# Optimization experiments

Hardware: AMD Instinct MI355X
Metric: run time of the kernel (lower is better)

Reference implementation:

```python
import jax, jax.numpy as jnp
import numpy as np

B, S, D = 4, 2048, 1024
DFF = 512
E = 16
TOP_K = 2
N_SHARED = 2
FUSED_DFF = DFF * N_SHARED


def setup_inputs() -> dict:
    key = jax.random.key(0)
    ks = jax.random.split(key, 16)
    sc_d = 1.0 / np.sqrt(D)
    sc_f = 1.0 / np.sqrt(DFF)
    sc_sf = 1.0 / np.sqrt(FUSED_DFF)
    inp = {
        "x": jax.random.normal(ks[0], (B, S, D), dtype=jnp.float32),
        "gate_w": jax.random.uniform(ks[1], (E, D), dtype=jnp.float32, minval=-sc_d, maxval=sc_d),
        "expert_bias": jnp.zeros((E,), dtype=jnp.float32),
        # routed experts (SwiGLU): w1,w3: [E, DFF, D], w2: [E, D, DFF]
        "w1": jax.random.uniform(ks[2], (E, DFF, D), dtype=jnp.float32, minval=-sc_d, maxval=sc_d),
        "b1": jax.random.uniform(ks[3], (E, DFF), dtype=jnp.float32, minval=-sc_d, maxval=sc_d),
        "w3": jax.random.uniform(ks[4], (E, DFF, D), dtype=jnp.float32, minval=-sc_d, maxval=sc_d),
        "b3": jax.random.uniform(ks[5], (E, DFF), dtype=jnp.float32, minval=-sc_d, maxval=sc_d),
        "w2": jax.random.uniform(ks[6], (E, D, DFF), dtype=jnp.float32, minval=-sc_f, maxval=sc_f),
        "b2": jax.random.uniform(ks[7], (E, D), dtype=jnp.float32, minval=-sc_f, maxval=sc_f),
        # fused shared experts: d_model -> 2*d_ff -> d_model
        "sw1": jax.random.uniform(ks[8], (FUSED_DFF, D), dtype=jnp.float32, minval=-sc_d, maxval=sc_d),
        "sb1": jax.random.uniform(ks[9], (FUSED_DFF,), dtype=jnp.float32, minval=-sc_d, maxval=sc_d),
        "sw3": jax.random.uniform(ks[10], (FUSED_DFF, D), dtype=jnp.float32, minval=-sc_d, maxval=sc_d),
        "sb3": jax.random.uniform(ks[11], (FUSED_DFF,), dtype=jnp.float32, minval=-sc_d, maxval=sc_d),
        "sw2": jax.random.uniform(ks[12], (D, FUSED_DFF), dtype=jnp.float32, minval=-sc_sf, maxval=sc_sf),
        "sb2": jax.random.uniform(ks[13], (D,), dtype=jnp.float32, minval=-sc_sf, maxval=sc_sf),
    }
    return inp


def reference(x, gate_w, expert_bias, w1, b1, w2, b2, w3, b3,
              sw1, sb1, sw2, sb2, sw3, sb3):
    Bv, Sv, Dv = x.shape
    xf = x.reshape(-1, Dv)                                  # [T, D]
    # --- Gate (sigmoid scores, top-k over bias-adjusted logits) ---
    logits = xf @ gate_w.T                                  # [T, E]
    scores = jax.nn.sigmoid(logits)
    biased = logits + expert_bias.astype(logits.dtype)[None, :]
    _, topk_idx = jax.lax.top_k(biased, TOP_K)              # [T, K]
    topk_w = jnp.take_along_axis(scores, topk_idx, axis=-1) # [T, K]
    topk_w = topk_w / (topk_w.sum(-1, keepdims=True) + 1e-10)
    # dense per-token per-expert combine weight (zero for unselected) [T, E]
    gatew = (jax.nn.one_hot(topk_idx, E, dtype=xf.dtype) * topk_w[..., None]).sum(1)
    # --- Routed experts: equivalent to sort/dispatch/grouped-GEMM/combine ---
    y = jnp.zeros_like(xf)
    for e in range(E):
        h = jax.nn.silu(xf @ w1[e].T + b1[e]) * (xf @ w3[e].T + b3[e])  # [T, DFF]
        y = y + gatew[:, e:e + 1] * (h @ w2[e].T + b2[e])
    # --- Fused shared experts ---
    hs = jax.nn.silu(xf @ sw1.T + sb1) * (xf @ sw3.T + sb3)             # [T, 2*DFF]
    y = y + hs @ sw2.T + sb2
    return y.reshape(Bv, Sv, Dv)
```

## Files before the change

kernel.cpp:

```cpp
#include <hip/hip_runtime.h>
#include <cstdint>
#include <cstddef>

#define DEV static __device__ __forceinline__

constexpr int TT   = 8192;
constexpr int DD   = 1024;
constexpr int DFF  = 512;
constexpr int NE   = 16;
constexpr int FDFF = 1024;
constexpr int NSLOT = TT * 2;
constexpr int NSLOT_PAD = NSLOT + NE * 128;
constexpr int MAXT = NSLOT / 128 + NE;
constexpr int HB   = 64;

constexpr size_t XB_OFF   = 0;
constexpr size_t HS_OFF   = XB_OFF  + (size_t)TT * DD * 2;
constexpr size_t HR_OFF   = HS_OFF  + (size_t)TT * FDFF * 2;
constexpr size_t YR_OFF   = HR_OFF  + (size_t)NSLOT_PAD * DFF * 2;
constexpr size_t W1B_OFF  = YR_OFF  + (size_t)NSLOT_PAD * DD * 2;
constexpr size_t W3B_OFF  = W1B_OFF + (size_t)NE * DFF * DD * 2;
constexpr size_t W2B_OFF  = W3B_OFF + (size_t)NE * DFF * DD * 2;
constexpr size_t SW1B_OFF = W2B_OFF + (size_t)NE * DD * DFF * 2;
constexpr size_t SW3B_OFF = SW1B_OFF + (size_t)FDFF * DD * 2;
constexpr size_t SW2B_OFF = SW3B_OFF + (size_t)FDFF * DD * 2;
constexpr size_t TKI_OFF  = SW2B_OFF + (size_t)DD * FDFF * 2;
constexpr size_t TKW_OFF  = TKI_OFF + (size_t)NSLOT * 4;
constexpr size_t STOK_OFF = TKW_OFF + (size_t)NSLOT * 4;
constexpr size_t TSL_OFF  = STOK_OFF + (size_t)NSLOT_PAD * 4;
constexpr size_t LRK_OFF  = TSL_OFF + (size_t)NSLOT * 4;
constexpr size_t BCN_OFF  = LRK_OFF + (size_t)NSLOT * 4;
constexpr size_t BB_OFF   = BCN_OFF + (size_t)HB * NE * 4;
constexpr size_t OFS_OFF  = BB_OFF + (size_t)HB * NE * 4;
constexpr size_t TEX_OFF  = OFS_OFF + 128;
constexpr size_t TM0_OFF  = TEX_OFF + (size_t)MAXT * 4;

typedef __bf16 bf16x8 __attribute__((ext_vector_type(8)));
typedef float  floatx4 __attribute__((ext_vector_type(4)));
typedef unsigned short u16t;

DEV unsigned f2bf2(float lo, float hi) {
    unsigned a = __builtin_bit_cast(unsigned, lo);
    unsigned b = __builtin_bit_cast(unsigned, hi);
    a += 0x7FFFu + ((a >> 16) & 1u);
    b += 0x7FFFu + ((b >> 16) & 1u);
    return (a >> 16) | (b & 0xFFFF0000u);
}
DEV u16t f2bf1(float f) {
    unsigned u = __builtin_bit_cast(unsigned, f);
    u += 0x7FFFu + ((u >> 16) & 1u);
    return (u16t)(u >> 16);
}
DEV float bf2f(u16t v) {
    return __builtin_bit_cast(float, ((unsigned)v) << 16);
}
DEV uint4 pack8(float4 a, float4 b) {
    uint4 r;
    r.x = f2bf2(a.x, a.y); r.y = f2bf2(a.z, a.w);
    r.z = f2bf2(b.x, b.y); r.w = f2bf2(b.z, b.w);
    return r;
}
DEV floatx4 mfma16(bf16x8 a, bf16x8 b, floatx4 c) {
    return __builtin_amdgcn_mfma_f32_16x16x32_bf16(a, b, c, 0, 0, 0);
}
DEV void glds16(const u16t* g, u16t* l) {
    __builtin_amdgcn_global_load_lds(
        (const __attribute__((address_space(1))) unsigned int*)g,
        (__attribute__((address_space(3))) unsigned int*)l, 16, 0, 0);
}
DEV float dot4(float4 a, float4 b) { return a.x*b.x + a.y*b.y + a.z*b.z + a.w*b.w; }

__global__ __launch_bounds__(256) void k_cvtw(
        const float* __restrict__ w1, const float* __restrict__ w3, const float* __restrict__ w2,
        const float* __restrict__ sw1, const float* __restrict__ sw3, const float* __restrict__ sw2,
        u16t* __restrict__ w1b, u16t* __restrict__ w3b, u16t* __restrict__ w2b,
        u16t* __restrict__ sw1b, u16t* __restrict__ sw3b, u16t* __restrict__ sw2b) {
    int b = blockIdx.x;
    const float* src; u16t* dst; size_t base;
    if      (b < 4096)  { src = w1;  dst = w1b;  base = (size_t)b * 2048; }
    else if (b < 8192)  { src = w3;  dst = w3b;  base = (size_t)(b - 4096) * 2048; }
    else if (b < 12288) { src = w2;  dst = w2b;  base = (size_t)(b - 8192) * 2048; }
    else if (b < 12800) { src = sw1; dst = sw1b; base = (size_t)(b - 12288) * 2048; }
    else if (b < 13312) { src = sw3; dst = sw3b; base = (size_t)(b - 12800) * 2048; }
    else                { src = sw2; dst = sw2b; base = (size_t)(b - 13312) * 2048; }
    size_t i = base + (size_t)threadIdx.x * 8;
    float4 a = *(const float4*)(src + i);
    float4 c = *(const float4*)(src + i + 4);
    *(uint4*)(dst + i) = pack8(a, c);
}

__global__ __launch_bounds__(256) void k_gate(const float* __restrict__ x,
                                              const float* __restrict__ gw,
                                              const float* __restrict__ eb,
                                              int* __restrict__ tki, float* __restrict__ tkw,
                                              u16t* __restrict__ xb) {
    const int tid = threadIdx.x;
    const int wave = tid >> 6, lane = tid & 63;
    const int tok0 = blockIdx.x * 16 + wave * 4;
    float acc[4][16];
#pragma unroll
    for (int t = 0; t < 4; t++)
#pragma unroll
        for (int e = 0; e < 16; e++) acc[t][e] = 0.f;
#pragma unroll
    for (int i = 0; i < 4; i++) {
        const int d = i * 256 + lane * 4;
        float4 xv[4];
#pragma unroll
        for (int t = 0; t < 4; t++) xv[t] = *(const float4*)(x + (size_t)(tok0 + t) * DD + d);
#pragma unroll
        for (int t = 0; t < 4; t++) {
            uint2 p;
            p.x = f2bf2(xv[t].x, xv[t].y);
            p.y = f2bf2(xv[t].z, xv[t].w);
            *(uint2*)(xb + (size_t)(tok0 + t) * DD + d) = p;
        }
#pragma unroll
        for (int e = 0; e < 16; e++) {
            float4 wv = *(const float4*)(gw + (size_t)e * DD + d);
#pragma unroll
            for (int t = 0; t < 4; t++) acc[t][e] += dot4(xv[t], wv);
        }
    }
#pragma unroll
    for (int t = 0; t < 4; t++)
#pragma unroll
        for (int e = 0; e < 16; e++) {
            float v = acc[t][e];
            v += __shfl_xor(v, 1);  v += __shfl_xor(v, 2);  v += __shfl_xor(v, 4);
            v += __shfl_xor(v, 8);  v += __shfl_xor(v, 16); v += __shfl_xor(v, 32);
            acc[t][e] = v;
        }
    if (lane == 0) {
        float ebs[16];
#pragma unroll
        for (int e = 0; e < 16; e++) ebs[e] = eb[e];
#pragma unroll
        for (int t = 0; t < 4; t++) {
            float b0 = -1e30f, b1v = -1e30f, l0 = 0.f, l1 = 0.f;
            int i0 = 0, i1 = 0;
#pragma unroll
            for (int e = 0; e < 16; e++) {
                float lv = acc[t][e];
                float bl = lv + ebs[e];
                if (bl > b0)       { b1v = b0; i1 = i0; l1 = l0; b0 = bl; i0 = e; l0 = lv; }
                else if (bl > b1v) { b1v = bl; i1 = e; l1 = lv; }
            }
            float s0 = 1.f / (1.f + expf(-l0));
            float s1 = 1.f / (1.f + expf(-l1));
            float dn = s0 + s1 + 1e-10f;
            int tok = tok0 + t;
            tki[tok * 2] = i0; tki[tok * 2 + 1] = i1;
            tkw[tok * 2] = s0 / dn; tkw[tok * 2 + 1] = s1 / dn;
        }
    }
}

__global__ __launch_bounds__(256) void k_hist(const int* __restrict__ tki,
                                              int* __restrict__ lrank, int* __restrict__ bcnt) {
    __shared__ int h[NE];
    const int tid = threadIdx.x;
    if (tid < NE) h[tid] = 0;
    __syncthreads();
    int idx = blockIdx.x * 256 + tid;
    int e = tki[idx];
    lrank[idx] = atomicAdd(&h[e], 1);
    __syncthreads();
    if (tid < NE) bcnt[blockIdx.x * NE + tid] = h[tid];
}

__global__ void k_scan(const int* __restrict__ bcnt, int* __restrict__ offs,
                       int* __restrict__ bb, int* __restrict__ texp, int* __restrict__ tm0) {
    __shared__ int cntS[NE], offS[NE];
    const int tid = threadIdx.x;
    if (tid < NE) {
        int s = 0;
#pragma unroll
        for (int b = 0; b < HB; b++) s += bcnt[b * NE + tid];
        cntS[tid] = s;
    }
    __syncthreads();
    if (tid == 0) {
        int off = 0, t = 0;
        for (int e = 0; e < NE; e++) {
            offS[e] = off; offs[e] = off;
            int nt = (cntS[e] + 127) >> 7;
            for (int i = 0; i < nt; i++) { texp[t] = e; tm0[t] = off + i * 128; t++; }
            off += nt * 128;
        }
        offs[NE] = off;
        for (; t < MAXT; t++) texp[t] = -1;
    }
    __syncthreads();
    if (tid < NE) {
        int run = offS[tid];
        for (int b = 0; b < HB; b++) { bb[b * NE + tid] = run; run += bcnt[b * NE + tid]; }
    }
}

__global__ __launch_bounds__(256) void k_scatter(const int* __restrict__ tki,
                                                 const int* __restrict__ bb,
                                                 const int* __restrict__ lrank,
                                                 int* __restrict__ stok,
                                                 int* __restrict__ tslot) {
    int idx = blockIdx.x * 256 + threadIdx.x;
    int e = tki[idx];
    int slot = bb[blockIdx.x * NE + e] + lrank[idx];
    stok[slot] = idx >> 1;
    tslot[idx] = slot;
}

__global__ __launch_bounds__(256) void k_sgemm1(const u16t* __restrict__ xb,
        const u16t* __restrict__ w1b, const float* __restrict__ sb1,
        const u16t* __restrict__ w3b, const float* __restrict__ sb3,
        u16t* __restrict__ Hs) {
    __shared__ u16t As[128 * 32], B1s[64 * 32], B3s[64 * 32];
    const int m0 = blockIdx.x * 128, n0 = blockIdx.y * 64;
    const int tid = threadIdx.x, lane = tid & 63, wid = tid >> 6;
    const int wm = (wid & 1) * 64, wn = (wid >> 1) * 32;
    const int q = lane >> 4, r = lane & 15;
    const int srow = tid >> 2, scg = (tid & 3) * 8;
    floatx4 acc1[4][2], acc3[4][2];
#pragma unroll
    for (int i = 0; i < 4; i++)
#pragma unroll
        for (int j = 0; j < 2; j++) { acc1[i][j] = (floatx4)0.f; acc3[i][j] = (floatx4)0.f; }
    const u16t* a0  = xb  + (size_t)(m0 + srow) * DD + scg;
    const u16t* a1  = xb  + (size_t)(m0 + 64 + srow) * DD + scg;
    const u16t* b1g = w1b + (size_t)(n0 + srow) * DD + scg;
    const u16t* b3g = w3b + (size_t)(n0 + srow) * DD + scg;
    u16t* lA0 = As + tid * 8;
    u16t* lA1 = As + 2048 + tid * 8;
    u16t* lB1 = B1s + tid * 8;
    u16t* lB3 = B3s + tid * 8;
    for (int k0 = 0; k0 < DD; k0 += 32) {
        glds16(a0 + k0, lA0); glds16(a1 + k0, lA1);
        glds16(b1g + k0, lB1); glds16(b3g + k0, lB3);
        __syncthreads();
        bf16x8 af[4], f1[2], f3[2];
#pragma unroll
        for (int i = 0; i < 4; i++) af[i] = *(const bf16x8*)&As[(wm + i * 16 + r) * 32 + q * 8];
#pragma unroll
        for (int j = 0; j < 2; j++) {
            f1[j] = *(const bf16x8*)&B1s[(wn + j * 16 + r) * 32 + q * 8];
            f3[j] = *(const bf16x8*)&B3s[(wn + j * 16 + r) * 32 + q * 8];
        }
#pragma unroll
        for (int i = 0; i < 4; i++)
#pragma unroll
            for (int j = 0; j < 2; j++) {
                acc1[i][j] = mfma16(af[i], f1[j], acc1[i][j]);
                acc3[i][j] = mfma16(af[i], f3[j], acc3[i][j]);
            }
        __syncthreads();
    }
    float s1v[2], s3v[2];
#pragma unroll
    for (int j = 0; j < 2; j++) {
        int col = n0 + wn + j * 16 + r;
        s1v[j] = sb1[col]; s3v[j] = sb3[col];
    }
#pragma unroll
    for (int i = 0; i < 4; i++)
#pragma unroll
        for (int j = 0; j < 2; j++)
#pragma unroll
            for (int g = 0; g < 4; g++) {
                int row = m0 + wm + i * 16 + q * 4 + g;
                int col = n0 + wn + j * 16 + r;
                float z1 = acc1[i][j][g] + s1v[j];
                float z3 = acc3[i][j][g] + s3v[j];
                float h = (z1 / (1.f + __expf(-z1))) * z3;
                Hs[(size_t)row * FDFF + col] = f2bf1(h);
            }
}

__global__ __launch_bounds__(256) void k_sgemm2(const u16t* __restrict__ Hs,
        const u16t* __restrict__ sw2b, const float* __restrict__ sb2,
        const u16t* __restrict__ Yr, const int* __restrict__ tslot,
        const float* __restrict__ tkw,
        float* __restrict__ out) {
    __shared__ u16t As[128 * 32], Bs[128 * 32];
    __shared__ int sl[256];
    __shared__ float wl[256];
    const int m0 = blockIdx.x * 128, n0 = blockIdx.y * 128;
    const int tid = threadIdx.x, lane = tid & 63, wid = tid >> 6;
    const int wm = (wid & 1) * 64, wn = (wid >> 1) * 64;
    const int q = lane >> 4, r = lane & 15;
    const int srow = tid >> 2, scg = (tid & 3) * 8;
    sl[tid] = tslot[m0 * 2 + tid];
    wl[tid] = tkw[m0 * 2 + tid];
    floatx4 acc[4][4];
#pragma unroll
    for (int i = 0; i < 4; i++)
#pragma unroll
        for (int j = 0; j < 4; j++) acc[i][j] = (floatx4)0.f;
    const u16t* a0 = Hs + (size_t)(m0 + srow) * FDFF + scg;
    const u16t* a1 = Hs + (size_t)(m0 + 64 + srow) * FDFF + scg;
    const u16t* b0 = sw2b + (size_t)(n0 + srow) * FDFF + scg;
    const u16t* b1 = sw2b + (size_t)(n0 + 64 + srow) * FDFF + scg;
    u16t* lA0 = As + tid * 8;       u16t* lA1 = As + 2048 + tid * 8;
    u16t* lB0 = Bs + tid * 8;       u16t* lB1 = Bs + 2048 + tid * 8;
    for (int k0 = 0; k0 < FDFF; k0 += 32) {
        glds16(a0 + k0, lA0); glds16(a1 + k0, lA1);
        glds16(b0 + k0, lB0); glds16(b1 + k0, lB1);
        __syncthreads();
        bf16x8 af[4], bf[4];
#pragma unroll
        for (int i = 0; i < 4; i++) af[i] = *(const bf16x8*)&As[(wm + i * 16 + r) * 32 + q * 8];
#pragma unroll
        for (int j = 0; j < 4; j++) bf[j] = *(const bf16x8*)&Bs[(wn + j * 16 + r) * 32 + q * 8];
#pragma unroll
        for (int i = 0; i < 4; i++)
#pragma unroll
            for (int j = 0; j < 4; j++) acc[i][j] = mfma16(af[i], bf[j], acc[i][j]);
        __syncthreads();
    }
    float bv[4];
#pragma unroll
    for (int j = 0; j < 4; j++) bv[j] = sb2[n0 + wn + j * 16 + r];
#pragma unroll
    for (int i = 0; i < 4; i++)
#pragma unroll
        for (int g = 0; g < 4; g++) {
            int rowl = wm + i * 16 + q * 4 + g;
            int s0 = sl[rowl * 2], s1 = sl[rowl * 2 + 1];
            float w0 = wl[rowl * 2], w1 = wl[rowl * 2 + 1];
            const u16t* y0p = Yr + (size_t)s0 * DD;
            const u16t* y1p = Yr + (size_t)s1 * DD;
#pragma unroll
            for (int j = 0; j < 4; j++) {
                int col = n0 + wn + j * 16 + r;
                float v = acc[i][j][g] + bv[j];
                v += w0 * bf2f(y0p[col]) + w1 * bf2f(y1p[col]);
                out[(size_t)(m0 + rowl) * DD + col] = v;
            }
        }
}

__global__ __launch_bounds__(256) void k_rgemm1(const u16t* __restrict__ xb,
        const u16t* __restrict__ w1b, const float* __restrict__ b1,
        const u16t* __restrict__ w3b, const float* __restrict__ b3,
        const int* __restrict__ stok,
        const int* __restrict__ texp, const int* __restrict__ tm0,
        u16t* __restrict__ Hr) {
    const int te = texp[blockIdx.x];
    if (te < 0) return;
    const int m0 = tm0[blockIdx.x], n0 = blockIdx.y * 64;
    __shared__ u16t As[128 * 32], B1s[64 * 32], B3s[64 * 32];
    __shared__ int toksS[128];
    const int tid = threadIdx.x, lane = tid & 63, wid = tid >> 6;
    const int wm = (wid & 1) * 64, wn = (wid >> 1) * 32;
    const int q = lane >> 4, r = lane & 15;
    const int srow = tid >> 2, scg = (tid & 3) * 8;
    if (tid < 128) { int t = stok[m0 + tid]; toksS[tid] = t < 0 ? 0 : t; }
    __syncthreads();
    floatx4 acc1[4][2], acc3[4][2];
#pragma unroll
    for (int i = 0; i < 4; i++)
#pragma unroll
        for (int j = 0; j < 2; j++) { acc1[i][j] = (floatx4)0.f; acc3[i][j] = (floatx4)0.f; }
    const u16t* a0  = xb + (size_t)toksS[srow] * DD + scg;
    const u16t* a1  = xb + (size_t)toksS[64 + srow] * DD + scg;
    const u16t* b1g = w1b + (size_t)te * DFF * DD + (size_t)(n0 + srow) * DD + scg;
    const u16t* b3g = w3b + (size_t)te * DFF * DD + (size_t)(n0 + srow) * DD + scg;
    const float* b1e = b1 + (size_t)te * DFF;
    const float* b3e = b3 + (size_t)te * DFF;
    u16t* lA0 = As + tid * 8;
    u16t* lA1 = As + 2048 + tid * 8;
    u16t* lB1 = B1s + tid * 8;
    u16t* lB3 = B3s + tid * 8;
    for (int k0 = 0; k0 < DD; k0 += 32) {
        glds16(a0 + k0, lA0); glds16(a1 + k0, lA1);
        glds16(b1g + k0, lB1); glds16(b3g + k0, lB3);
        __syncthreads();
        bf16x8 af[4], f1[2], f3[2];
#pragma unroll
        for (int i = 0; i < 4; i++) af[i] = *(const bf16x8*)&As[(wm + i * 16 + r) * 32 + q * 8];
#pragma unroll
        for (int j = 0; j < 2; j++) {
            f1[j] = *(const bf16x8*)&B1s[(wn + j * 16 + r) * 32 + q * 8];
            f3[j] = *(const bf16x8*)&B3s[(wn + j * 16 + r) * 32 + q * 8];
        }
#pragma unroll
        for (int i = 0; i < 4; i++)
#pragma unroll
            for (int j = 0; j < 2; j++) {
                acc1[i][j] = mfma16(af[i], f1[j], acc1[i][j]);
                acc3[i][j] = mfma16(af[i], f3[j], acc3[i][j]);
            }
        __syncthreads();
    }
    float s1v[2], s3v[2];
#pragma unroll
    for (int j = 0; j < 2; j++) {
        int col = n0 + wn + j * 16 + r;
        s1v[j] = b1e[col]; s3v[j] = b3e[col];
    }
#pragma unroll
    for (int i = 0; i < 4; i++)
#pragma unroll
        for (int j = 0; j < 2; j++)
#pragma unroll
            for (int g = 0; g < 4; g++) {
                int slot = m0 + wm + i * 16 + q * 4 + g;
                int col = n0 + wn + j * 16 + r;
                float z1 = acc1[i][j][g] + s1v[j];
                float z3 = acc3[i][j][g] + s3v[j];
                float h = (z1 / (1.f + __expf(-z1))) * z3;
                Hr[(size_t)slot * DFF + col] = f2bf1(h);
            }
}

__global__ __launch_bounds__(256) void k_rgemm2(const u16t* __restrict__ Hr,
        const u16t* __restrict__ w2b, const float* __restrict__ b2,
        const int* __restrict__ texp, const int* __restrict__ tm0,
        u16t* __restrict__ Yr) {
    const int te = texp[blockIdx.x];
    if (te < 0) return;
    const int m0 = tm0[blockIdx.x], n0 = blockIdx.y * 128;
    __shared__ u16t As[128 * 32], Bs[128 * 32];
    const int tid = threadIdx.x, lane = tid & 63, wid = tid >> 6;
    const int wm = (wid & 1) * 64, wn = (wid >> 1) * 64;
    const int q = lane >> 4, r = lane & 15;
    const int srow = tid >> 2, scg = (tid & 3) * 8;
    floatx4 acc[4][4];
#pragma unroll
    for (int i = 0; i < 4; i++)
#pragma unroll
        for (int j = 0; j < 4; j++) acc[i][j] = (floatx4)0.f;
    const u16t* a0 = Hr + (size_t)(m0 + srow) * DFF + scg;
    const u16t* a1 = Hr + (size_t)(m0 + 64 + srow) * DFF + scg;
    const u16t* b0 = w2b + (size_t)te * DD * DFF + (size_t)(n0 + srow) * DFF + scg;
    const u16t* b1 = w2b + (size_t)te * DD * DFF + (size_t)(n0 + 64 + srow) * DFF + scg;
    const float* b2e = b2 + (size_t)te * DD;
    u16t* lA0 = As + tid * 8;       u16t* lA1 = As + 2048 + tid * 8;
    u16t* lB0 = Bs + tid * 8;       u16t* lB1 = Bs + 2048 + tid * 8;
    for (int k0 = 0; k0 < DFF; k0 += 32) {
        glds16(a0 + k0, lA0); glds16(a1 + k0, lA1);
        glds16(b0 + k0, lB0); glds16(b1 + k0, lB1);
        __syncthreads();
        bf16x8 af[4], bf[4];
#pragma unroll
        for (int i = 0; i < 4; i++) af[i] = *(const bf16x8*)&As[(wm + i * 16 + r) * 32 + q * 8];
#pragma unroll
        for (int j = 0; j < 4; j++) bf[j] = *(const bf16x8*)&Bs[(wn + j * 16 + r) * 32 + q * 8];
#pragma unroll
        for (int i = 0; i < 4; i++)
#pragma unroll
            for (int j = 0; j < 4; j++) acc[i][j] = mfma16(af[i], bf[j], acc[i][j]);
        __syncthreads();
    }
    float bv[4];
#pragma unroll
    for (int j = 0; j < 4; j++) bv[j] = b2e[n0 + wn + j * 16 + r];
#pragma unroll
    for (int i = 0; i < 4; i++)
#pragma unroll
        for (int g = 0; g < 4; g++) {
            int slot = m0 + wm + i * 16 + q * 4 + g;
#pragma unroll
            for (int j = 0; j < 4; j++) {
                int col = n0 + wn + j * 16 + r;
                Yr[(size_t)slot * DD + col] = f2bf1(acc[i][j][g] + bv[j]);
            }
        }
}

extern "C" void kernel_launch(void* const* d_in, const int* in_sizes, int n_in,
                              void* d_out, int out_size, void* d_ws, size_t ws_size,
                              hipStream_t stream) {
    const float* x   = (const float*)d_in[0];
    const float* gw  = (const float*)d_in[1];
    const float* eb  = (const float*)d_in[2];
    const float* w1  = (const float*)d_in[3];
    const float* b1  = (const float*)d_in[4];
    const float* w3  = (const float*)d_in[5];
    const float* b3  = (const float*)d_in[6];
    const float* w2  = (const float*)d_in[7];
    const float* b2  = (const float*)d_in[8];
    const float* sw1 = (const float*)d_in[9];
    const float* sb1 = (const float*)d_in[10];
    const float* sw3 = (const float*)d_in[11];
    const float* sb3 = (const float*)d_in[12];
    const float* sw2 = (const float*)d_in[13];
    const float* sb2 = (const float*)d_in[14];
    float* out = (float*)d_out;
    char* ws = (char*)d_ws;

    u16t*  xb   = (u16t*)(ws + XB_OFF);
    u16t*  Hs   = (u16t*)(ws + HS_OFF);
    u16t*  Hr   = (u16t*)(ws + HR_OFF);
    u16t*  Yr   = (u16t*)(ws + YR_OFF);
    u16t*  w1b  = (u16t*)(ws + W1B_OFF);
    u16t*  w3b  = (u16t*)(ws + W3B_OFF);
    u16t*  w2b  = (u16t*)(ws + W2B_OFF);
    u16t*  sw1b = (u16t*)(ws + SW1B_OFF);
    u16t*  sw3b = (u16t*)(ws + SW3B_OFF);
    u16t*  sw2b = (u16t*)(ws + SW2B_OFF);
    int*   tki  = (int*)(ws + TKI_OFF);
    float* tkw  = (float*)(ws + TKW_OFF);
    int*   stok = (int*)(ws + STOK_OFF);
    int*   tslot = (int*)(ws + TSL_OFF);
    int*   lrank = (int*)(ws + LRK_OFF);
    int*   bcnt = (int*)(ws + BCN_OFF);
    int*   bb   = (int*)(ws + BB_OFF);
    int*   offs = (int*)(ws + OFS_OFF);
    int*   texp = (int*)(ws + TEX_OFF);
    int*   tm0  = (int*)(ws + TM0_OFF);

    hipMemsetAsync(stok, 0xFF, (size_t)NSLOT_PAD * 4, stream);

    k_cvtw<<<13824, 256, 0, stream>>>(w1, w3, w2, sw1, sw3, sw2, w1b, w3b, w2b, sw1b, sw3b, sw2b);
    k_gate<<<512, 256, 0, stream>>>(x, gw, eb, tki, tkw, xb);
    k_hist<<<HB, 256, 0, stream>>>(tki, lrank, bcnt);
    k_scan<<<1, 64, 0, stream>>>(bcnt, offs, bb, texp, tm0);
    k_scatter<<<HB, 256, 0, stream>>>(tki, bb, lrank, stok, tslot);

    k_rgemm1<<<dim3(MAXT, DFF / 64), 256, 0, stream>>>(xb, w1b, b1, w3b, b3, stok, texp, tm0, Hr);
    k_rgemm2<<<dim3(MAXT, DD / 128), 256, 0, stream>>>(Hr, w2b, b2, texp, tm0, Yr);

    k_sgemm1<<<dim3(TT / 128, FDFF / 64), 256, 0, stream>>>(xb, sw1b, sb1, sw3b, sb3, Hs);
    k_sgemm2<<<dim3(TT / 128, DD / 128), 256, 0, stream>>>(Hs, sw2b, sb2, Yr, tslot, tkw, out);
}
```

Before: 416.6 us.

## Double-buffer LDS tiles in all four expert GEMM kernels

Each of the shared and routed GEMM kernels now uses two LDS buffers. The next K-slice is loaded directly to LDS while the MFMAs run on the current one, which halves the barriers per K step and overlaps global load latency with compute. The routed first GEMM also reads token indices straight into registers instead of staging them in LDS behind a barrier. LDS use per block doubles, which may lower occupancy. Correctness depends on the async global-to-LDS loads having completed at the barrier.

```diff
diff --git a/kernel.cpp b/kernel.cpp
--- a/kernel.cpp
+++ b/kernel.cpp
@@ -210,11 +210,12 @@
     tslot[idx] = slot;
 }
 
+
 __global__ __launch_bounds__(256) void k_sgemm1(const u16t* __restrict__ xb,
         const u16t* __restrict__ w1b, const float* __restrict__ sb1,
         const u16t* __restrict__ w3b, const float* __restrict__ sb3,
         u16t* __restrict__ Hs) {
-    __shared__ u16t As[128 * 32], B1s[64 * 32], B3s[64 * 32];
+    __shared__ u16t As[2][128 * 32], B1s[2][64 * 32], B3s[2][64 * 32];
     const int m0 = blockIdx.x * 128, n0 = blockIdx.y * 64;
     const int tid = threadIdx.x, lane = tid & 63, wid = tid >> 6;
     const int wm = (wid & 1) * 64, wn = (wid >> 1) * 32;
@@ -229,31 +230,43 @@
     const u16t* a1  = xb  + (size_t)(m0 + 64 + srow) * DD + scg;
     const u16t* b1g = w1b + (size_t)(n0 + srow) * DD + scg;
     const u16t* b3g = w3b + (size_t)(n0 + srow) * DD + scg;
-    u16t* lA0 = As + tid * 8;
-    u16t* lA1 = As + 2048 + tid * 8;
-    u16t* lB1 = B1s + tid * 8;
-    u16t* lB3 = B3s + tid * 8;
-    for (int k0 = 0; k0 < DD; k0 += 32) {
-        glds16(a0 + k0, lA0); glds16(a1 + k0, lA1);
-        glds16(b1g + k0, lB1); glds16(b3g + k0, lB3);
-        __syncthreads();
-        bf16x8 af[4], f1[2], f3[2];
-#pragma unroll
-        for (int i = 0; i < 4; i++) af[i] = *(const bf16x8*)&As[(wm + i * 16 + r) * 32 + q * 8];
-#pragma unroll
-        for (int j = 0; j < 2; j++) {
-            f1[j] = *(const bf16x8*)&B1s[(wn + j * 16 + r) * 32 + q * 8];
-            f3[j] = *(const bf16x8*)&B3s[(wn + j * 16 + r) * 32 + q * 8];
-        }
-#pragma unroll
-        for (int i = 0; i < 4; i++)
-#pragma unroll
-            for (int j = 0; j < 2; j++) {
-                acc1[i][j] = mfma16(af[i], f1[j], acc1[i][j]);
-                acc3[i][j] = mfma16(af[i], f3[j], acc3[i][j]);
-            }
-        __syncthreads();
-    }
+
+#define SG1_STAGE(bf, kk) do { \
+        glds16(a0 + (kk), &As[bf][tid * 8]); \
+        glds16(a1 + (kk), &As[bf][2048 + tid * 8]); \
+        glds16(b1g + (kk), &B1s[bf][tid * 8]); \
+        glds16(b3g + (kk), &B3s[bf][tid * 8]); \
+    } while (0)
+#define SG1_COMP(bf) do { \
+        bf16x8 af[4], f1[2], f3[2]; \
+        _Pragma("unroll") \
+        for (int i = 0; i < 4; i++) af[i] = *(const bf16x8*)&As[bf][(wm + i * 16 + r) * 32 + q * 8]; \
+        _Pragma("unroll") \
+        for (int j = 0; j < 2; j++) { \
+            f1[j] = *(const bf16x8*)&B1s[bf][(wn + j * 16 + r) * 32 + q * 8]; \
+            f3[j] = *(const bf16x8*)&B3s[bf][(wn + j * 16 + r) * 32 + q * 8]; \
+        } \
+        _Pragma("unroll") \
+        for (int i = 0; i < 4; i++) \
+            _Pragma("unroll") \
+            for (int j = 0; j < 2; j++) { \
+                acc1[i][j] = mfma16(af[i], f1[j], acc1[i][j]); \
+                acc3[i][j] = mfma16(af[i], f3[j], acc3[i][j]); \
+            } \
+    } while (0)
+
+    SG1_STAGE(0, 0);
+    __syncthreads();
+    for (int k0 = 0; k0 + 64 <= DD; k0 += 64) {
+        SG1_STAGE(1, k0 + 32);
+        SG1_COMP(0);
+        __syncthreads();
+        if (k0 + 64 < DD) SG1_STAGE(0, k0 + 64);
+        SG1_COMP(1);
+        __syncthreads();
+    }
+#undef SG1_STAGE
+#undef SG1_COMP
     float s1v[2], s3v[2];
 #pragma unroll
     for (int j = 0; j < 2; j++) {
@@ -280,7 +293,7 @@
         const u16t* __restrict__ Yr, const int* __restrict__ tslot,
         const float* __restrict__ tkw,
         float* __restrict__ out) {
-    __shared__ u16t As[128 * 32], Bs[128 * 32];
+    __shared__ u16t As[2][128 * 32], Bs[2][128 * 32];
     __shared__ int sl[256];
     __shared__ float wl[256];
     const int m0 = blockIdx.x * 128, n0 = blockIdx.y * 128;
@@ -299,23 +312,37 @@
     const u16t* a1 = Hs + (size_t)(m0 + 64 + srow) * FDFF + scg;
     const u16t* b0 = sw2b + (size_t)(n0 + srow) * FDFF + scg;
     const u16t* b1 = sw2b + (size_t)(n0 + 64 + srow) * FDFF + scg;
-    u16t* lA0 = As + tid * 8;       u16t* lA1 = As + 2048 + tid * 8;
-    u16t* lB0 = Bs + tid * 8;       u16t* lB1 = Bs + 2048 + tid * 8;
-    for (int k0 = 0; k0 < FDFF; k0 += 32) {
-        glds16(a0 + k0, lA0); glds16(a1 + k0, lA1);
-        glds16(b0 + k0, lB0); glds16(b1 + k0, lB1);
-        __syncthreads();
-        bf16x8 af[4], bf[4];
-#pragma unroll
-        for (int i = 0; i < 4; i++) af[i] = *(const bf16x8*)&As[(wm + i * 16 + r) * 32 + q * 8];
-#pragma unroll
-        for (int j = 0; j < 4; j++) bf[j] = *(const bf16x8*)&Bs[(wn + j * 16 + r) * 32 + q * 8];
-#pragma unroll
-        for (int i = 0; i < 4; i++)
-#pragma unroll
-            for (int j = 0; j < 4; j++) acc[i][j] = mfma16(af[i], bf[j], acc[i][j]);
-        __syncthreads();
-    }
+
+#define SG2_STAGE(bf, kk) do { \
+        glds16(a0 + (kk), &As[bf][tid * 8]); \
+        glds16(a1 + (kk), &As[bf][2048 + tid * 8]); \
+        glds16(b0 + (kk), &Bs[bf][tid * 8]); \
+        glds16(b1 + (kk), &Bs[bf][2048 + tid * 8]); \
+    } while (0)
+#define SG2_COMP(bf) do { \
+        bf16x8 af[4], bfr[4]; \
+        _Pragma("unroll") \
+        for (int i = 0; i < 4; i++) af[i] = *(const bf16x8*)&As[bf][(wm + i * 16 + r) * 32 + q * 8]; \
+        _Pragma("unroll") \
+        for (int j = 0; j < 4; j++) bfr[j] = *(const bf16x8*)&Bs[bf][(wn + j * 16 + r) * 32 + q * 8]; \
+        _Pragma("unroll") \
+        for (int i = 0; i < 4; i++) \
+            _Pragma("unroll") \
+            for (int j = 0; j < 4; j++) acc[i][j] = mfma16(af[i], bfr[j], acc[i][j]); \
+    } while (0)
+
+    SG2_STAGE(0, 0);
+    __syncthreads();
+    for (int k0 = 0; k0 + 64 <= FDFF; k0 += 64) {
+        SG2_STAGE(1, k0 + 32);
+        SG2_COMP(0);
+        __syncthreads();
+        if (k0 + 64 < FDFF) SG2_STAGE(0, k0 + 64);
+        SG2_COMP(1);
+        __syncthreads();
+    }
+#undef SG2_STAGE
+#undef SG2_COMP
     float bv[4];
 #pragma unroll
     for (int j = 0; j < 4; j++) bv[j] = sb2[n0 + wn + j * 16 + r];
@@ -347,50 +374,61 @@
     const int te = texp[blockIdx.x];
     if (te < 0) return;
     const int m0 = tm0[blockIdx.x], n0 = blockIdx.y * 64;
-    __shared__ u16t As[128 * 32], B1s[64 * 32], B3s[64 * 32];
-    __shared__ int toksS[128];
+    __shared__ u16t As[2][128 * 32], B1s[2][64 * 32], B3s[2][64 * 32];
     const int tid = threadIdx.x, lane = tid & 63, wid = tid >> 6;
     const int wm = (wid & 1) * 64, wn = (wid >> 1) * 32;
     const int q = lane >> 4, r = lane & 15;
     const int srow = tid >> 2, scg = (tid & 3) * 8;
-    if (tid < 128) { int t = stok[m0 + tid]; toksS[tid] = t < 0 ? 0 : t; }
-    __syncthreads();
+    int t0 = stok[m0 + srow];       if (t0 < 0) t0 = 0;
+    int t1 = stok[m0 + 64 + srow];  if (t1 < 0) t1 = 0;
     floatx4 acc1[4][2], acc3[4][2];
 #pragma unroll
     for (int i = 0; i < 4; i++)
 #pragma unroll
         for (int j = 0; j < 2; j++) { acc1[i][j] = (floatx4)0.f; acc3[i][j] = (floatx4)0.f; }
-    const u16t* a0  = xb + (size_t)toksS[srow] * DD + scg;
-    const u16t* a1  = xb + (size_t)toksS[64 + srow] * DD + scg;
+    const u16t* a0  = xb + (size_t)t0 * DD + scg;
+    const u16t* a1  = xb + (size_t)t1 * DD + scg;
     const u16t* b1g = w1b + (size_t)te * DFF * DD + (size_t)(n0 + srow) * DD + scg;
     const u16t* b3g = w3b + (size_t)te * DFF * DD + (size_t)(n0 + srow) * DD + scg;
     const float* b1e = b1 + (size_t)te * DFF;
     const float* b3e = b3 + (size_t)te * DFF;
-    u16t* lA0 = As + tid * 8;
-    u16t* lA1 = As + 2048 + tid * 8;
-    u16t* lB1 = B1s + tid * 8;
-    u16t* lB3 = B3s + tid * 8;
-    for (int k0 = 0; k0 < DD; k0 += 32) {
-        glds16(a0 + k0, lA0); glds16(a1 + k0, lA1);
-        glds16(b1g + k0, lB1); glds16(b3g + k0, lB3);
-        __syncthreads();
-        bf16x8 af[4], f1[2], f3[2];
-#pragma unroll
-        for (int i = 0; i < 4; i++) af[i] = *(const bf16x8*)&As[(wm + i * 16 + r) * 32 + q * 8];
-#pragma unroll
-        for (int j = 0; j < 2; j++) {
-            f1[j] = *(const bf16x8*)&B1s[(wn + j * 16 + r) * 32 + q * 8];
-            f3[j] = *(const bf16x8*)&B3s[(wn + j * 16 + r) * 32 + q * 8];
-        }
-#pragma unroll
-        for (int i = 0; i < 4; i++)
-#pragma unroll
-            for (int j = 0; j < 2; j++) {
-                acc1[i][j] = mfma16(af[i], f1[j], acc1[i][j]);
-                acc3[i][j] = mfma16(af[i], f3[j], acc3[i][j]);
-            }
-        __syncthreads();
-    }
+
+#define RG1_STAGE(bf, kk) do { \
+        glds16(a0 + (kk), &As[bf][tid * 8]); \
+        glds16(a1 + (kk), &As[bf][2048 + tid * 8]); \
+        glds16(b1g + (kk), &B1s[bf][tid * 8]); \
+        glds16(b3g + (kk), &B3s[bf][tid * 8]); \
+    } while (0)
+#define RG1_COMP(bf) do { \
+        bf16x8 af[4], f1[2], f3[2]; \
+        _Pragma("unroll") \
+        for (int i = 0; i < 4; i++) af[i] = *(const bf16x8*)&As[bf][(wm + i * 16 + r) * 32 + q * 8]; \
+        _Pragma("unroll") \
+        for (int j = 0; j < 2; j++) { \
+            f1[j] = *(const bf16x8*)&B1s[bf][(wn + j * 16 + r) * 32 + q * 8]; \
+            f3[j] = *(const bf16x8*)&B3s[bf][(wn + j * 16 + r) * 32 + q * 8]; \
+        } \
+        _Pragma("unroll") \
+        for (int i = 0; i < 4; i++) \
+            _Pragma("unroll") \
+            for (int j = 0; j < 2; j++) { \
+                acc1[i][j] = mfma16(af[i], f1[j], acc1[i][j]); \
+                acc3[i][j] = mfma16(af[i], f3[j], acc3[i][j]); \
+            } \
+    } while (0)
+
+    RG1_STAGE(0, 0);
+    __syncthreads();
+    for (int k0 = 0; k0 + 64 <= DD; k0 += 64) {
+        RG1_STAGE(1, k0 + 32);
+        RG1_COMP(0);
+        __syncthreads();
+        if (k0 + 64 < DD) RG1_STAGE(0, k0 + 64);
+        RG1_COMP(1);
+        __syncthreads();
+    }
+#undef RG1_STAGE
+#undef RG1_COMP
     float s1v[2], s3v[2];
 #pragma unroll
     for (int j = 0; j < 2; j++) {
@@ -419,7 +457,7 @@
     const int te = texp[blockIdx.x];
     if (te < 0) return;
     const int m0 = tm0[blockIdx.x], n0 = blockIdx.y * 128;
-    __shared__ u16t As[128 * 32], Bs[128 * 32];
+    __shared__ u16t As[2][128 * 32], Bs[2][128 * 32];
     const int tid = threadIdx.x, lane = tid & 63, wid = tid >> 6;
     const int wm = (wid & 1) * 64, wn = (wid >> 1) * 64;
     const int q = lane >> 4, r = lane & 15;
@@ -434,23 +472,37 @@
     const u16t* b0 = w2b + (size_t)te * DD * DFF + (size_t)(n0 + srow) * DFF + scg;
     const u16t* b1 = w2b + (size_t)te * DD * DFF + (size_t)(n0 + 64 + srow) * DFF + scg;
     const float* b2e = b2 + (size_t)te * DD;
-    u16t* lA0 = As + tid * 8;       u16t* lA1 = As + 2048 + tid * 8;
-    u16t* lB0 = Bs + tid * 8;       u16t* lB1 = Bs + 2048 + tid * 8;
-    for (int k0 = 0; k0 < DFF; k0 += 32) {
-        glds16(a0 + k0, lA0); glds16(a1 + k0, lA1);
-        glds16(b0 + k0, lB0); glds16(b1 + k0, lB1);
-        __syncthreads();
-        bf16x8 af[4], bf[4];
-#pragma unroll
-        for (int i = 0; i < 4; i++) af[i] = *(const bf16x8*)&As[(wm + i * 16 + r) * 32 + q * 8];
-#pragma unroll
-        for (int j = 0; j < 4; j++) bf[j] = *(const bf16x8*)&Bs[(wn + j * 16 + r) * 32 + q * 8];
-#pragma unroll
-        for (int i = 0; i < 4; i++)
-#pragma unroll
-            for (int j = 0; j < 4; j++) acc[i][j] = mfma16(af[i], bf[j], acc[i][j]);
-        __syncthreads();
-    }
+
+#define RG2_STAGE(bf, kk) do { \
+        glds16(a0 + (kk), &As[bf][tid * 8]); \
+        glds16(a1 + (kk), &As[bf][2048 + tid * 8]); \
+        glds16(b0 + (kk), &Bs[bf][tid * 8]); \
+        glds16(b1 + (kk), &Bs[bf][2048 + tid * 8]); \
+    } while (0)
+#define RG2_COMP(bf) do { \
+        bf16x8 af[4], bfr[4]; \
+        _Pragma("unroll") \
+        for (int i = 0; i < 4; i++) af[i] = *(const bf16x8*)&As[bf][(wm + i * 16 + r) * 32 + q * 8]; \
+        _Pragma("unroll") \
+        for (int j = 0; j < 4; j++) bfr[j] = *(const bf16x8*)&Bs[bf][(wn + j * 16 + r) * 32 + q * 8]; \
+        _Pragma("unroll") \
+        for (int i = 0; i < 4; i++) \
+            _Pragma("unroll") \
+            for (int j = 0; j < 4; j++) acc[i][j] = mfma16(af[i], bfr[j], acc[i][j]); \
+    } while (0)
+
+    RG2_STAGE(0, 0);
+    __syncthreads();
+    for (int k0 = 0; k0 + 64 <= DFF; k0 += 64) {
+        RG2_STAGE(1, k0 + 32);
+        RG2_COMP(0);
+        __syncthreads();
+        if (k0 + 64 < DFF) RG2_STAGE(0, k0 + 64);
+        RG2_COMP(1);
+        __syncthreads();
+    }
+#undef RG2_STAGE
+#undef RG2_COMP
     float bv[4];
 #pragma unroll
     for (int j = 0; j < 4; j++) bv[j] = b2e[n0 + wn + j * 16 + r];
```

After: 420.7 us. No clear change (+1.0%).

## Merge routed and shared first GEMMs into one launch with XCD-aware block swizzle

Applied to the files above, without the earlier changes.

Combines the routed-expert and shared-expert up-projection GEMMs into a single kernel with a flattened 1D grid, so padding-tile early exits and tail effects are absorbed by the other workload. It also remaps block indices across the 8 XCDs in all three GEMMs so that blocks sharing weight or activation tiles run on the same XCD and reuse its L2. The routed path now loads token indices directly instead of staging them in shared memory. The cost is branch setup per block and a fixed swizzle that assumes grid sizes divisible by 8.

```diff
diff --git a/kernel.cpp b/kernel.cpp
--- a/kernel.cpp
+++ b/kernel.cpp
@@ -13,6 +13,12 @@
 constexpr int NSLOT_PAD = NSLOT + NE * 128;
 constexpr int MAXT = NSLOT / 128 + NE;
 constexpr int HB   = 64;
+
+constexpr int RB1 = MAXT * (DFF / 64);
+constexpr int SB1 = (TT / 128) * (FDFF / 64);
+constexpr int NB1 = RB1 + SB1;
+constexpr int NB_RG2 = MAXT * (DD / 128);
+constexpr int NB_SG2 = (TT / 128) * (DD / 128);
 
 constexpr size_t XB_OFF   = 0;
 constexpr size_t HS_OFF   = XB_OFF  + (size_t)TT * DD * 2;
@@ -210,32 +216,62 @@
     tslot[idx] = slot;
 }
 
-__global__ __launch_bounds__(256) void k_sgemm1(const u16t* __restrict__ xb,
-        const u16t* __restrict__ w1b, const float* __restrict__ sb1,
-        const u16t* __restrict__ w3b, const float* __restrict__ sb3,
-        u16t* __restrict__ Hs) {
+__global__ __launch_bounds__(256) void k_gemm1(const u16t* __restrict__ xb,
+        const u16t* __restrict__ w1b, const float* __restrict__ b1,
+        const u16t* __restrict__ w3b, const float* __restrict__ b3,
+        const u16t* __restrict__ sw1b, const float* __restrict__ sb1,
+        const u16t* __restrict__ sw3b, const float* __restrict__ sb3,
+        const int* __restrict__ stok,
+        const int* __restrict__ texp, const int* __restrict__ tm0,
+        u16t* __restrict__ Hr, u16t* __restrict__ Hs) {
     __shared__ u16t As[128 * 32], B1s[64 * 32], B3s[64 * 32];
-    const int m0 = blockIdx.x * 128, n0 = blockIdx.y * 64;
     const int tid = threadIdx.x, lane = tid & 63, wid = tid >> 6;
     const int wm = (wid & 1) * 64, wn = (wid >> 1) * 32;
     const int q = lane >> 4, r = lane & 15;
     const int srow = tid >> 2, scg = (tid & 3) * 8;
+
+    const int swz = ((int)blockIdx.x & 7) * (NB1 / 8) + ((int)blockIdx.x >> 3);
+    const u16t *a0, *a1, *bg1, *bg3;
+    const float *bs1, *bs3;
+    u16t* hout; int m0, n0, ostr;
+    if (swz < RB1) {
+        const int mt = swz >> 3, nb = swz & 7;
+        const int te = texp[mt];
+        if (te < 0) return;
+        m0 = tm0[mt]; n0 = nb * 64;
+        int t0 = stok[m0 + srow];      if (t0 < 0) t0 = 0;
+        int t1 = stok[m0 + 64 + srow]; if (t1 < 0) t1 = 0;
+        a0 = xb + (size_t)t0 * DD + scg;
+        a1 = xb + (size_t)t1 * DD + scg;
+        bg1 = w1b + (size_t)te * DFF * DD + (size_t)(n0 + srow) * DD + scg;
+        bg3 = w3b + (size_t)te * DFF * DD + (size_t)(n0 + srow) * DD + scg;
+        bs1 = b1 + (size_t)te * DFF;
+        bs3 = b3 + (size_t)te * DFF;
+        hout = Hr; ostr = DFF;
+    } else {
+        const int s = swz - RB1;
+        const int mt = s >> 4, nb = s & 15;
+        m0 = mt * 128; n0 = nb * 64;
+        a0 = xb + (size_t)(m0 + srow) * DD + scg;
+        a1 = xb + (size_t)(m0 + 64 + srow) * DD + scg;
+        bg1 = sw1b + (size_t)(n0 + srow) * DD + scg;
+        bg3 = sw3b + (size_t)(n0 + srow) * DD + scg;
+        bs1 = sb1; bs3 = sb3;
+        hout = Hs; ostr = FDFF;
+    }
+
     floatx4 acc1[4][2], acc3[4][2];
 #pragma unroll
     for (int i = 0; i < 4; i++)
 #pragma unroll
         for (int j = 0; j < 2; j++) { acc1[i][j] = (floatx4)0.f; acc3[i][j] = (floatx4)0.f; }
-    const u16t* a0  = xb  + (size_t)(m0 + srow) * DD + scg;
-    const u16t* a1  = xb  + (size_t)(m0 + 64 + srow) * DD + scg;
-    const u16t* b1g = w1b + (size_t)(n0 + srow) * DD + scg;
-    const u16t* b3g = w3b + (size_t)(n0 + srow) * DD + scg;
     u16t* lA0 = As + tid * 8;
     u16t* lA1 = As + 2048 + tid * 8;
     u16t* lB1 = B1s + tid * 8;
     u16t* lB3 = B3s + tid * 8;
     for (int k0 = 0; k0 < DD; k0 += 32) {
         glds16(a0 + k0, lA0); glds16(a1 + k0, lA1);
-        glds16(b1g + k0, lB1); glds16(b3g + k0, lB3);
+        glds16(bg1 + k0, lB1); glds16(bg3 + k0, lB3);
         __syncthreads();
         bf16x8 af[4], f1[2], f3[2];
 #pragma unroll
@@ -258,7 +294,7 @@
 #pragma unroll
     for (int j = 0; j < 2; j++) {
         int col = n0 + wn + j * 16 + r;
-        s1v[j] = sb1[col]; s3v[j] = sb3[col];
+        s1v[j] = bs1[col]; s3v[j] = bs3[col];
     }
 #pragma unroll
     for (int i = 0; i < 4; i++)
@@ -271,144 +307,7 @@
                 float z1 = acc1[i][j][g] + s1v[j];
                 float z3 = acc3[i][j][g] + s3v[j];
                 float h = (z1 / (1.f + __expf(-z1))) * z3;
-                Hs[(size_t)row * FDFF + col] = f2bf1(h);
-            }
-}
-
-__global__ __launch_bounds__(256) void k_sgemm2(const u16t* __restrict__ Hs,
-        const u16t* __restrict__ sw2b, const float* __restrict__ sb2,
-        const u16t* __restrict__ Yr, const int* __restrict__ tslot,
-        const float* __restrict__ tkw,
-        float* __restrict__ out) {
-    __shared__ u16t As[128 * 32], Bs[128 * 32];
-    __shared__ int sl[256];
-    __shared__ float wl[256];
-    const int m0 = blockIdx.x * 128, n0 = blockIdx.y * 128;
-    const int tid = threadIdx.x, lane = tid & 63, wid = tid >> 6;
-    const int wm = (wid & 1) * 64, wn = (wid >> 1) * 64;
-    const int q = lane >> 4, r = lane & 15;
-    const int srow = tid >> 2, scg = (tid & 3) * 8;
-    sl[tid] = tslot[m0 * 2 + tid];
-    wl[tid] = tkw[m0 * 2 + tid];
-    floatx4 acc[4][4];
-#pragma unroll
-    for (int i = 0; i < 4; i++)
-#pragma unroll
-        for (int j = 0; j < 4; j++) acc[i][j] = (floatx4)0.f;
-    const u16t* a0 = Hs + (size_t)(m0 + srow) * FDFF + scg;
-    const u16t* a1 = Hs + (size_t)(m0 + 64 + srow) * FDFF + scg;
-    const u16t* b0 = sw2b + (size_t)(n0 + srow) * FDFF + scg;
-    const u16t* b1 = sw2b + (size_t)(n0 + 64 + srow) * FDFF + scg;
-    u16t* lA0 = As + tid * 8;       u16t* lA1 = As + 2048 + tid * 8;
-    u16t* lB0 = Bs + tid * 8;       u16t* lB1 = Bs + 2048 + tid * 8;
-    for (int k0 = 0; k0 < FDFF; k0 += 32) {
-        glds16(a0 + k0, lA0); glds16(a1 + k0, lA1);
-        glds16(b0 + k0, lB0); glds16(b1 + k0, lB1);
-        __syncthreads();
-        bf16x8 af[4], bf[4];
-#pragma unroll
-        for (int i = 0; i < 4; i++) af[i] = *(const bf16x8*)&As[(wm + i * 16 + r) * 32 + q * 8];
-#pragma unroll
-        for (int j = 0; j < 4; j++) bf[j] = *(const bf16x8*)&Bs[(wn + j * 16 + r) * 32 + q * 8];
-#pragma unroll
-        for (int i = 0; i < 4; i++)
-#pragma unroll
-            for (int j = 0; j < 4; j++) acc[i][j] = mfma16(af[i], bf[j], acc[i][j]);
-        __syncthreads();
-    }
-    float bv[4];
-#pragma unroll
-    for (int j = 0; j < 4; j++) bv[j] = sb2[n0 + wn + j * 16 + r];
-#pragma unroll
-    for (int i = 0; i < 4; i++)
-#pragma unroll
-        for (int g = 0; g < 4; g++) {
-            int rowl = wm + i * 16 + q * 4 + g;
-            int s0 = sl[rowl * 2], s1 = sl[rowl * 2 + 1];
-            float w0 = wl[rowl * 2], w1 = wl[rowl * 2 + 1];
-            const u16t* y0p = Yr + (size_t)s0 * DD;
-            const u16t* y1p = Yr + (size_t)s1 * DD;
-#pragma unroll
-            for (int j = 0; j < 4; j++) {
-                int col = n0 + wn + j * 16 + r;
-                float v = acc[i][j][g] + bv[j];
-                v += w0 * bf2f(y0p[col]) + w1 * bf2f(y1p[col]);
-                out[(size_t)(m0 + rowl) * DD + col] = v;
-            }
-        }
-}
-
-__global__ __launch_bounds__(256) void k_rgemm1(const u16t* __restrict__ xb,
-        const u16t* __restrict__ w1b, const float* __restrict__ b1,
-        const u16t* __restrict__ w3b, const float* __restrict__ b3,
-        const int* __restrict__ stok,
-        const int* __restrict__ texp, const int* __restrict__ tm0,
-        u16t* __restrict__ Hr) {
-    const int te = texp[blockIdx.x];
-    if (te < 0) return;
-    const int m0 = tm0[blockIdx.x], n0 = blockIdx.y * 64;
-    __shared__ u16t As[128 * 32], B1s[64 * 32], B3s[64 * 32];
-    __shared__ int toksS[128];
-    const int tid = threadIdx.x, lane = tid & 63, wid = tid >> 6;
-    const int wm = (wid & 1) * 64, wn = (wid >> 1) * 32;
-    const int q = lane >> 4, r = lane & 15;
-    const int srow = tid >> 2, scg = (tid & 3) * 8;
-    if (tid < 128) { int t = stok[m0 + tid]; toksS[tid] = t < 0 ? 0 : t; }
-    __syncthreads();
-    floatx4 acc1[4][2], acc3[4][2];
-#pragma unroll
-    for (int i = 0; i < 4; i++)
-#pragma unroll
-        for (int j = 0; j < 2; j++) { acc1[i][j] = (floatx4)0.f; acc3[i][j] = (floatx4)0.f; }
-    const u16t* a0  = xb + (size_t)toksS[srow] * DD + scg;
-    const u16t* a1  = xb + (size_t)toksS[64 + srow] * DD + scg;
-    const u16t* b1g = w1b + (size_t)te * DFF * DD + (size_t)(n0 + srow) * DD + scg;
-    const u16t* b3g = w3b + (size_t)te * DFF * DD + (size_t)(n0 + srow) * DD + scg;
-    const float* b1e = b1 + (size_t)te * DFF;
-    const float* b3e = b3 + (size_t)te * DFF;
-    u16t* lA0 = As + tid * 8;
-    u16t* lA1 = As + 2048 + tid * 8;
-    u16t* lB1 = B1s + tid * 8;
-    u16t* lB3 = B3s + tid * 8;
-    for (int k0 = 0; k0 < DD; k0 += 32) {
-        glds16(a0 + k0, lA0); glds16(a1 + k0, lA1);
-        glds16(b1g + k0, lB1); glds16(b3g + k0, lB3);
-        __syncthreads();
-        bf16x8 af[4], f1[2], f3[2];
-#pragma unroll
-        for (int i = 0; i < 4; i++) af[i] = *(const bf16x8*)&As[(wm + i * 16 + r) * 32 + q * 8];
-#pragma unroll
-        for (int j = 0; j < 2; j++) {
-            f1[j] = *(const bf16x8*)&B1s[(wn + j * 16 + r) * 32 + q * 8];
-            f3[j] = *(const bf16x8*)&B3s[(wn + j * 16 + r) * 32 + q * 8];
-        }
-#pragma unroll
-        for (int i = 0; i < 4; i++)
-#pragma unroll
-            for (int j = 0; j < 2; j++) {
-                acc1[i][j] = mfma16(af[i], f1[j], acc1[i][j]);
-                acc3[i][j] = mfma16(af[i], f3[j], acc3[i][j]);
-            }
-        __syncthreads();
-    }
-    float s1v[2], s3v[2];
-#pragma unroll
-    for (int j = 0; j < 2; j++) {
-        int col = n0 + wn + j * 16 + r;
-        s1v[j] = b1e[col]; s3v[j] = b3e[col];
-    }
-#pragma unroll
-    for (int i = 0; i < 4; i++)
-#pragma unroll
-        for (int j = 0; j < 2; j++)
-#pragma unroll
-            for (int g = 0; g < 4; g++) {
-                int slot = m0 + wm + i * 16 + q * 4 + g;
-                int col = n0 + wn + j * 16 + r;
-                float z1 = acc1[i][j][g] + s1v[j];
-                float z3 = acc3[i][j][g] + s3v[j];
-                float h = (z1 / (1.f + __expf(-z1))) * z3;
-                Hr[(size_t)slot * DFF + col] = f2bf1(h);
+                hout[(size_t)row * ostr + col] = f2bf1(h);
             }
 }
 
@@ -416,9 +315,11 @@
         const u16t* __restrict__ w2b, const float* __restrict__ b2,
         const int* __restrict__ texp, const int* __restrict__ tm0,
         u16t* __restrict__ Yr) {
-    const int te = texp[blockIdx.x];
+    const int swz = ((int)blockIdx.x & 7) * (NB_RG2 / 8) + ((int)blockIdx.x >> 3);
+    const int mt = swz >> 3, nb = swz & 7;
+    const int te = texp[mt];
     if (te < 0) return;
-    const int m0 = tm0[blockIdx.x], n0 = blockIdx.y * 128;
+    const int m0 = tm0[mt], n0 = nb * 128;
     __shared__ u16t As[128 * 32], Bs[128 * 32];
     const int tid = threadIdx.x, lane = tid & 63, wid = tid >> 6;
     const int wm = (wid & 1) * 64, wn = (wid >> 1) * 64;
@@ -463,6 +364,71 @@
             for (int j = 0; j < 4; j++) {
                 int col = n0 + wn + j * 16 + r;
                 Yr[(size_t)slot * DD + col] = f2bf1(acc[i][j][g] + bv[j]);
+            }
+        }
+}
+
+__global__ __launch_bounds__(256) void k_sgemm2(const u16t* __restrict__ Hs,
+        const u16t* __restrict__ sw2b, const float* __restrict__ sb2,
+        const u16t* __restrict__ Yr, const int* __restrict__ tslot,
+        const float* __restrict__ tkw,
+        float* __restrict__ out) {
+    const int swz = ((int)blockIdx.x & 7) * (NB_SG2 / 8) + ((int)blockIdx.x >> 3);
+    const int mt = swz >> 3, nb = swz & 7;
+    const int m0 = mt * 128, n0 = nb * 128;
+    __shared__ u16t As[128 * 32], Bs[128 * 32];
+    __shared__ int sl[256];
+    __shared__ float wl[256];
+    const int tid = threadIdx.x, lane = tid & 63, wid = tid >> 6;
+    const int wm = (wid & 1) * 64, wn = (wid >> 1) * 64;
+    const int q = lane >> 4, r = lane & 15;
+    const int srow = tid >> 2, scg = (tid & 3) * 8;
+    sl[tid] = tslot[m0 * 2 + tid];
+    wl[tid] = tkw[m0 * 2 + tid];
+    floatx4 acc[4][4];
+#pragma unroll
+    for (int i = 0; i < 4; i++)
+#pragma unroll
+        for (int j = 0; j < 4; j++) acc[i][j] = (floatx4)0.f;
+    const u16t* a0 = Hs + (size_t)(m0 + srow) * FDFF + scg;
+    const u16t* a1 = Hs + (size_t)(m0 + 64 + srow) * FDFF + scg;
+    const u16t* b0 = sw2b + (size_t)(n0 + srow) * FDFF + scg;
+    const u16t* b1 = sw2b + (size_t)(n0 + 64 + srow) * FDFF + scg;
+    u16t* lA0 = As + tid * 8;       u16t* lA1 = As + 2048 + tid * 8;
+    u16t* lB0 = Bs + tid * 8;       u16t* lB1 = Bs + 2048 + tid * 8;
+    for (int k0 = 0; k0 < FDFF; k0 += 32) {
+        glds16(a0 + k0, lA0); glds16(a1 + k0, lA1);
+        glds16(b0 + k0, lB0); glds16(b1 + k0, lB1);
+        __syncthreads();
+        bf16x8 af[4], bf[4];
+#pragma unroll
+        for (int i = 0; i < 4; i++) af[i] = *(const bf16x8*)&As[(wm + i * 16 + r) * 32 + q * 8];
+#pragma unroll
+        for (int j = 0; j < 4; j++) bf[j] = *(const bf16x8*)&Bs[(wn + j * 16 + r) * 32 + q * 8];
+#pragma unroll
+        for (int i = 0; i < 4; i++)
+#pragma unroll
+            for (int j = 0; j < 4; j++) acc[i][j] = mfma16(af[i], bf[j], acc[i][j]);
+        __syncthreads();
+    }
+    float bv[4];
+#pragma unroll
+    for (int j = 0; j < 4; j++) bv[j] = sb2[n0 + wn + j * 16 + r];
+#pragma unroll
+    for (int i = 0; i < 4; i++)
+#pragma unroll
+        for (int g = 0; g < 4; g++) {
+            int rowl = wm + i * 16 + q * 4 + g;
+            int s0 = sl[rowl * 2], s1 = sl[rowl * 2 + 1];
+            float w0 = wl[rowl * 2], w1 = wl[rowl * 2 + 1];
+            const u16t* y0p = Yr + (size_t)s0 * DD;
+            const u16t* y1p = Yr + (size_t)s1 * DD;
+#pragma unroll
+            for (int j = 0; j < 4; j++) {
+                int col = n0 + wn + j * 16 + r;
+                float v = acc[i][j][g] + bv[j];
+                v += w0 * bf2f(y0p[col]) + w1 * bf2f(y1p[col]);
+                out[(size_t)(m0 + rowl) * DD + col] = v;
             }
         }
 }
@@ -517,9 +483,8 @@
     k_scan<<<1, 64, 0, stream>>>(bcnt, offs, bb, texp, tm0);
     k_scatter<<<HB, 256, 0, stream>>>(tki, bb, lrank, stok, tslot);
 
-    k_rgemm1<<<dim3(MAXT, DFF / 64), 256, 0, stream>>>(xb, w1b, b1, w3b, b3, stok, texp, tm0, Hr);
-    k_rgemm2<<<dim3(MAXT, DD / 128), 256, 0, stream>>>(Hr, w2b, b2, texp, tm0, Yr);
-
-    k_sgemm1<<<dim3(TT / 128, FDFF / 64), 256, 0, stream>>>(xb, sw1b, sb1, sw3b, sb3, Hs);
-    k_sgemm2<<<dim3(TT / 128, DD / 128), 256, 0, stream>>>(Hs, sw2b, sb2, Yr, tslot, tkw, out);
-}
+    k_gemm1<<<NB1, 256, 0, stream>>>(xb, w1b, b1, w3b, b3, sw1b, sb1, sw3b, sb3,
+                                     stok, texp, tm0, Hr, Hs);
+    k_rgemm2<<<NB_RG2, 256, 0, stream>>>(Hr, w2b, b2, texp, tm0, Yr);
+    k_sgemm2<<<NB_SG2, 256, 0, stream>>>(Hs, sw2b, sb2, Yr, tslot, tkw, out);
+}
```

Measured after the change: 385.9 us. -7.4%, faster.
